# Performance work log

Hardware: AMD Instinct MI355X
Metric: run time of the kernel (lower is better)

Reference implementation:

```python
import jax, jax.numpy as jnp
import numpy as np

B, N, HID, H = 16, 256, 512, 8
DK = HID // H          # att_size = 64
FEAT = 8               # storage/operator feature dim
MLP_H = 64             # interaction MLP hidden dim
LAM = 0.1              # htap_lambda
SCALE = DK ** -0.5


def _pair_bias(feat, W1, b1, W2, b2):
    """MLP([v_i || v_j || |v_i - v_j|]) for all pairs -> [B,N,N,H].
    Split W1 over the three concat blocks so the per-node parts are O(N)."""
    F = feat.shape[-1]
    Wa, Wb, Wc = W1[:F], W1[F:2 * F], W1[2 * F:]
    hi = feat @ Wa                                    # [B,N,MLP_H]
    hj = feat @ Wb                                    # [B,N,MLP_H]
    diff = jnp.abs(feat[:, :, None, :] - feat[:, None, :, :])  # [B,N,N,F]
    h = jax.nn.relu(hi[:, :, None, :] + hj[:, None, :, :] + diff @ Wc + b1)
    return h @ W2 + b2                                # [B,N,N,H]


def setup_inputs() -> dict:
    key = jax.random.key(0)
    ks = jax.random.split(key, 24)
    g = lambda i, shape, s=0.05: jax.random.normal(ks[i], shape, jnp.float32) * (1.0 if s is None else 1.0) * (s / 0.05 * 0.05 if False else 1.0)
    def w(i, shape, scale):
        return jax.random.normal(ks[i], shape, jnp.float32) * scale
    inp = {
        "q": w(0, (B, N, HID), 1.0),
        "k": w(1, (B, N, HID), 1.0),
        "v": w(2, (B, N, HID), 1.0),
        "tree_attn_bias": w(3, (B, H, N, N), 1.0),
        "storage_features": w(4, (B, N, FEAT), 1.0),
        "operator_features": w(5, (B, N, FEAT), 1.0),
        # attention projections (stored as [in,out])
        "Wq": w(6, (HID, HID), HID ** -0.5), "bq": jnp.zeros((HID,), jnp.float32),
        "Wk": w(7, (HID, HID), HID ** -0.5), "bk": jnp.zeros((HID,), jnp.float32),
        "Wv": w(8, (HID, HID), HID ** -0.5), "bv": jnp.zeros((HID,), jnp.float32),
        "Wo": w(9, (HID, HID), HID ** -0.5), "bo": jnp.zeros((HID,), jnp.float32),
        # f_s interaction MLP: Linear(3*FEAT,64) -> ReLU -> Linear(64,H)
        "fs_W1": w(10, (3 * FEAT, MLP_H), (3 * FEAT) ** -0.5), "fs_b1": jnp.zeros((MLP_H,), jnp.float32),
        "fs_W2": w(11, (MLP_H, H), MLP_H ** -0.5), "fs_b2": jnp.zeros((H,), jnp.float32),
        # f_o interaction MLP
        "fo_W1": w(12, (3 * FEAT, MLP_H), (3 * FEAT) ** -0.5), "fo_b1": jnp.zeros((MLP_H,), jnp.float32),
        "fo_W2": w(13, (MLP_H, H), MLP_H ** -0.5), "fo_b2": jnp.zeros((H,), jnp.float32),
    }
    return inp


def reference(q, k, v, tree_attn_bias, storage_features, operator_features,
              Wq, bq, Wk, bk, Wv, bv, Wo, bo,
              fs_W1, fs_b1, fs_W2, fs_b2, fo_W1, fo_b1, fo_W2, fo_b2):
    # projections -> [B,H,N,DK]
    qh = (q @ Wq + bq).reshape(B, N, H, DK).transpose(0, 2, 1, 3) * SCALE
    kh = (k @ Wk + bk).reshape(B, N, H, DK).transpose(0, 2, 1, 3)
    vh = (v @ Wv + bv).reshape(B, N, H, DK).transpose(0, 2, 1, 3)

    scores = jnp.einsum("bhnd,bhmd->bhnm", qh, kh) + tree_attn_bias

    htap = (_pair_bias(storage_features, fs_W1, fs_b1, fs_W2, fs_b2)
            + _pair_bias(operator_features, fo_W1, fo_b1, fo_W2, fo_b2))  # [B,N,N,H]
    scores = scores + LAM * htap.transpose(0, 3, 1, 2)

    attn = jax.nn.softmax(scores, axis=-1)            # dropout rate 0 (eval)
    x = jnp.einsum("bhnm,bhmd->bhnd", attn, vh)
    x = x.transpose(0, 2, 1, 3).reshape(B, N, HID)
    return x @ Wo + bo
```

## Files before the change

### kernel.cpp

```cpp
#include <hip/hip_runtime.h>
#include <hip/hip_bf16.h>
#include <stdint.h>

#define B_    16
#define N_    256
#define HID_  512
#define H_    8
#define DK_   64
#define FEAT_ 8
#define MLPH_ 64
#define LAM_  0.1f
#define SCALE_ 0.125f

typedef short bf16x8 __attribute__((ext_vector_type(8)));
typedef float f32x4  __attribute__((ext_vector_type(4)));

union U8 { uint4 u; bf16x8 h; ushort s[8]; };

__device__ __forceinline__ uint16_t f32_to_bf16(float x) {
    uint32_t u = __float_as_uint(x);
    u += 0x7fffu + ((u >> 16) & 1u);
    return (uint16_t)(u >> 16);
}
__device__ __forceinline__ float bf16_to_f32(uint16_t v) {
    return __uint_as_float(((uint32_t)v) << 16);
}
__device__ __forceinline__ uint32_t pk_bf16(float lo, float hi) {
    float2 xy; xy.x = lo; xy.y = hi;
    __hip_bfloat162 b2 = __float22bfloat162_rn(xy);
    return *(uint32_t*)&b2;
}
#define LDS_FENCE() asm volatile("s_waitcnt lgkmcnt(0)" ::: "memory")

__global__ __launch_bounds__(256) void cvt_prep(
    const float* __restrict__ q, const float* __restrict__ k, const float* __restrict__ v,
    const float* __restrict__ Wq, const float* __restrict__ Wk,
    const float* __restrict__ Wv, const float* __restrict__ Wo,
    const float* __restrict__ fsW1, const float* __restrict__ foW1,
    const float* __restrict__ fsW2, const float* __restrict__ foW2,
    ushort* __restrict__ qb, ushort* __restrict__ kb, ushort* __restrict__ vb,
    ushort* __restrict__ Wqt, ushort* __restrict__ Wkt,
    ushort* __restrict__ Wvt, ushort* __restrict__ Wot,
    uint4* __restrict__ bfrag1, uint4* __restrict__ bfrag2)
{
    __shared__ float tile[64][65];
    int t = threadIdx.x;
    int z = blockIdx.y, bx = blockIdx.x;

    if (z < 3) {
        const float* src = (z == 0) ? q : (z == 1) ? k : v;
        ushort* dst      = (z == 0) ? qb : (z == 1) ? kb : vb;
        size_t base = (size_t)bx * 2048 + (size_t)t * 8;
        float4 a = *(const float4*)&src[base];
        float4 b = *(const float4*)&src[base + 4];
        uint4 o;
        o.x = pk_bf16(a.x, a.y); o.y = pk_bf16(a.z, a.w);
        o.z = pk_bf16(b.x, b.y); o.w = pk_bf16(b.z, b.w);
        *(uint4*)&dst[base] = o;
        return;
    }

    if (bx < 256) {
        int mat = bx >> 6, tl = bx & 63;
        const float* Wf = (mat == 0) ? Wq : (mat == 1) ? Wk : (mat == 2) ? Wv : Wo;
        ushort* Wt      = (mat == 0) ? Wqt : (mat == 1) ? Wkt : (mat == 2) ? Wvt : Wot;
        int ki0 = (tl >> 3) * 64, ni0 = (tl & 7) * 64;
        {
            int r = t >> 2, cq = (t & 3) * 16;
            #pragma unroll
            for (int j = 0; j < 4; j++) {
                float4 v4 = *(const float4*)&Wf[(ki0 + r) * HID_ + ni0 + cq + j * 4];
                tile[r][cq + j * 4 + 0] = v4.x; tile[r][cq + j * 4 + 1] = v4.y;
                tile[r][cq + j * 4 + 2] = v4.z; tile[r][cq + j * 4 + 3] = v4.w;
            }
        }
        __syncthreads();
        {
            int n = t >> 2, kq = (t & 3) * 16;
            uint4 o0, o1;
            o0.x = pk_bf16(tile[kq + 0][n], tile[kq + 1][n]);
            o0.y = pk_bf16(tile[kq + 2][n], tile[kq + 3][n]);
            o0.z = pk_bf16(tile[kq + 4][n], tile[kq + 5][n]);
            o0.w = pk_bf16(tile[kq + 6][n], tile[kq + 7][n]);
            o1.x = pk_bf16(tile[kq + 8][n], tile[kq + 9][n]);
            o1.y = pk_bf16(tile[kq + 10][n], tile[kq + 11][n]);
            o1.z = pk_bf16(tile[kq + 12][n], tile[kq + 13][n]);
            o1.w = pk_bf16(tile[kq + 14][n], tile[kq + 15][n]);
            *(uint4*)&Wt[(ni0 + n) * HID_ + ki0 + kq] = o0;
            *(uint4*)&Wt[(ni0 + n) * HID_ + ki0 + kq + 8] = o1;
        }
        return;
    }

    if (bx == 256) {
        #pragma unroll
        for (int e = t; e < 512; e += 256) {
            int nt = e >> 6, lane = e & 63, l15 = lane & 15, qd = lane >> 4;
            int n = nt * 16 + l15;
            ushort vals[8];
            #pragma unroll
            for (int u = 0; u < 8; u++) {
                float x = 0.f;
                if (n < 64) {
                    if (qd == 0) x = fsW1[(16 + u) * 64 + n];
                    else if (qd == 1) x = fsW1[(8 + u) * 64 + n];
                } else {
                    int n2 = n - 64;
                    if (qd == 2) x = foW1[(16 + u) * 64 + n2];
                    else if (qd == 3) x = foW1[(8 + u) * 64 + n2];
                }
                vals[u] = f32_to_bf16(x);
            }
            uint4 pk;
            pk.x = (uint32_t)vals[0] | ((uint32_t)vals[1] << 16);
            pk.y = (uint32_t)vals[2] | ((uint32_t)vals[3] << 16);
            pk.z = (uint32_t)vals[4] | ((uint32_t)vals[5] << 16);
            pk.w = (uint32_t)vals[6] | ((uint32_t)vals[7] << 16);
            bfrag1[e] = pk;
        }
        {
            int e = t;
            int ks = e >> 6, lane = e & 63, l15 = lane & 15, qd = lane >> 4;
            ushort vals[8];
            #pragma unroll
            for (int u = 0; u < 8; u++) {
                float x = 0.f;
                if (l15 < 8) {
                    int k2 = ks * 32 + qd * 8 + u;
                    int c = ((k2 & 7) << 4) | (k2 >> 3);
                    x = LAM_ * ((c < 64) ? fsW2[c * 8 + l15] : foW2[(c - 64) * 8 + l15]);
                }
                vals[u] = f32_to_bf16(x);
            }
            uint4 pk;
            pk.x = (uint32_t)vals[0] | ((uint32_t)vals[1] << 16);
            pk.y = (uint32_t)vals[2] | ((uint32_t)vals[3] << 16);
            pk.z = (uint32_t)vals[4] | ((uint32_t)vals[5] << 16);
            pk.w = (uint32_t)vals[6] | ((uint32_t)vals[7] << 16);
            bfrag2[e] = pk;
        }
    }
}

__global__ __launch_bounds__(256, 4) void proj_kernel(
    const ushort* __restrict__ qb, const ushort* __restrict__ kb, const ushort* __restrict__ vb,
    const ushort* __restrict__ Wqt, const ushort* __restrict__ Wkt, const ushort* __restrict__ Wvt,
    const float* __restrict__ bq, const float* __restrict__ bk, const float* __restrict__ bv,
    ushort* __restrict__ qh, ushort* __restrict__ kh, ushort* __restrict__ vh)
{
    int z = blockIdx.z;
    const ushort* X   = (z == 0) ? qb  : (z == 1) ? kb  : vb;
    const ushort* Wt  = (z == 0) ? Wqt : (z == 1) ? Wkt : Wvt;
    const float* bias = (z == 0) ? bq  : (z == 1) ? bk  : bv;
    ushort* out       = (z == 0) ? qh  : (z == 1) ? kh  : vh;
    float scale       = (z == 0) ? SCALE_ : 1.0f;

    int m0 = blockIdx.x * 128;
    int h  = blockIdx.y;
    int c0 = h * 64;

    __shared__ __align__(16) ushort Xs[2][128 * 40];
    __shared__ __align__(16) ushort Ws[2][64 * 40];

    int t = threadIdx.x;
    int wave = t >> 6, lane = t & 63;
    int l15 = lane & 15, qd = lane >> 4;

    int xr = t >> 1, xc = (t & 1) * 16;
    int wn = t >> 2, wk = (t & 3) * 8;

    f32x4 acc0[4] = {}, acc1[4] = {};

    uint4 xv0, xv1, wv;
    xv0 = *(const uint4*)&X[(size_t)(m0 + xr) * HID_ + xc];
    xv1 = *(const uint4*)&X[(size_t)(m0 + xr) * HID_ + xc + 8];
    wv  = *(const uint4*)&Wt[(size_t)(c0 + wn) * HID_ + wk];

    for (int k0 = 0; k0 < HID_; k0 += 32) {
        int buf = (k0 >> 5) & 1;
        *(uint4*)&Xs[buf][xr * 40 + xc]     = xv0;
        *(uint4*)&Xs[buf][xr * 40 + xc + 8] = xv1;
        *(uint4*)&Ws[buf][wn * 40 + wk]     = wv;
        __syncthreads();

        if (k0 + 32 < HID_) {
            int kn = k0 + 32;
            xv0 = *(const uint4*)&X[(size_t)(m0 + xr) * HID_ + kn + xc];
            xv1 = *(const uint4*)&X[(size_t)(m0 + xr) * HID_ + kn + xc + 8];
            wv  = *(const uint4*)&Wt[(size_t)(c0 + wn) * HID_ + kn + wk];
        }

        bf16x8 af0 = *(const bf16x8*)&Xs[buf][(wave * 32 + l15) * 40 + qd * 8];
        bf16x8 af1 = *(const bf16x8*)&Xs[buf][(wave * 32 + 16 + l15) * 40 + qd * 8];
        #pragma unroll
        for (int nt = 0; nt < 4; nt++) {
            bf16x8 bf = *(const bf16x8*)&Ws[buf][(nt * 16 + l15) * 40 + qd * 8];
            acc0[nt] = __builtin_amdgcn_mfma_f32_16x16x32_bf16(af0, bf, acc0[nt], 0, 0, 0);
            acc1[nt] = __builtin_amdgcn_mfma_f32_16x16x32_bf16(af1, bf, acc1[nt], 0, 0, 0);
        }
    }

    #pragma unroll
    for (int nt = 0; nt < 4; nt++) {
        float bb = bias[c0 + nt * 16 + l15];
        #pragma unroll
        for (int g = 0; g < 2; g++) {
            const f32x4& a = g ? acc1[nt] : acc0[nt];
            #pragma unroll
            for (int r = 0; r < 4; r++) {
                int m = m0 + wave * 32 + g * 16 + qd * 4 + r;
                int b_ = m >> 8, n_ = m & 255;
                float val = (a[r] + bb) * scale;
                out[(((b_ * H_ + h) * N_) + n_) * DK_ + nt * 16 + l15] = f32_to_bf16(val);
            }
        }
    }
}

#define HSTRIDE 136
__global__ __launch_bounds__(256, 3) void pair_bias_mfma(
    const float* __restrict__ sf, const float* __restrict__ of,
    const float* __restrict__ fsW1, const float* __restrict__ fsb1,
    const float* __restrict__ foW1, const float* __restrict__ fob1,
    const float* __restrict__ fsb2, const float* __restrict__ fob2,
    const uint4* __restrict__ bfrag1, const uint4* __restrict__ bfrag2,
    ushort* __restrict__ mlpb)
{
    __shared__ __align__(16) ushort hbuf[4][2][16 * HSTRIDE];
    __shared__ float hisbuf[128];
    __shared__ __align__(16) ushort mout[8 * 16 * 24];

    int i = blockIdx.x, b = blockIdx.y;
    int t = threadIdx.x;
    int wave = t >> 6, lane = t & 63;
    int l15 = lane & 15, qd = lane >> 4;

    if (t < 128) {
        int set = t >> 6, kk = t & 63;
        const float* W1 = set ? foW1 : fsW1;
        const float* fi = (set ? of : sf) + (b * N_ + i) * FEAT_;
        float a = (set ? fob1 : fsb1)[kk];
        #pragma unroll
        for (int f = 0; f < FEAT_; f++) a += fi[f] * W1[f * 64 + kk];
        hisbuf[t] = a;
    }

    bf16x8 Bf1[8], Bf2[4];
    #pragma unroll
    for (int nt = 0; nt < 8; nt++) { U8 u; u.u = bfrag1[nt * 64 + lane]; Bf1[nt] = u.h; }
    #pragma unroll
    for (int ks = 0; ks < 4; ks++) { U8 u; u.u = bfrag2[ks * 64 + lane]; Bf2[ks] = u.h; }

    const float* fsr = sf + (b * N_ + i) * FEAT_;
    const float* forr = of + (b * N_ + i) * FEAT_;
    float fsi[8], foi[8];
    #pragma unroll
    for (int u = 0; u < 8; u++) { fsi[u] = fsr[u]; foi[u] = forr[u]; }
    float b2l = LAM_ * (fsb2[l15 & 7] + fob2[l15 & 7]);

    bf16x8 af[4];
    #pragma unroll
    for (int qt = 0; qt < 4; qt++) {
        int j = (wave * 4 + qt) * 16 + l15;
        const float* fr = ((qd < 2) ? sf : of) + (b * N_ + j) * FEAT_;
        float4 f0 = *(const float4*)&fr[0];
        float4 f1 = *(const float4*)&fr[4];
        float vals[8] = {f0.x, f0.y, f0.z, f0.w, f1.x, f1.y, f1.z, f1.w};
        if ((qd & 1) == 0) {
            const float* fi = (qd < 2) ? fsi : foi;
            #pragma unroll
            for (int u = 0; u < 8; u++) vals[u] = fabsf(vals[u] - fi[u]);
        }
        U8 au;
        #pragma unroll
        for (int p = 0; p < 4; p++)
            ((uint32_t*)&au)[p] = pk_bf16(vals[2 * p], vals[2 * p + 1]);
        af[qt] = au.h;
    }

    __syncthreads();
    float hv[8];
    #pragma unroll
    for (int nt = 0; nt < 8; nt++) hv[nt] = hisbuf[nt * 16 + l15];

    {
        f32x4 S1[8];
        #pragma unroll
        for (int nt = 0; nt < 8; nt++) {
            f32x4 c0 = {hv[nt], hv[nt], hv[nt], hv[nt]};
            S1[nt] = __builtin_amdgcn_mfma_f32_16x16x32_bf16(af[0], Bf1[nt], c0, 0, 0, 0);
        }
        ushort* hb = &hbuf[wave][0][0];
        #pragma unroll
        for (int r = 0; r < 4; r++) {
            uint4 w;
            w.x = pk_bf16(fmaxf(S1[0][r], 0.f), fmaxf(S1[1][r], 0.f));
            w.y = pk_bf16(fmaxf(S1[2][r], 0.f), fmaxf(S1[3][r], 0.f));
            w.z = pk_bf16(fmaxf(S1[4][r], 0.f), fmaxf(S1[5][r], 0.f));
            w.w = pk_bf16(fmaxf(S1[6][r], 0.f), fmaxf(S1[7][r], 0.f));
            *(uint4*)&hb[(qd * 4 + r) * HSTRIDE + l15 * 8] = w;
        }
    }

    #pragma unroll
    for (int qt = 0; qt < 4; qt++) {
        ushort* hbC = &hbuf[wave][qt & 1][0];
        ushort* hbN = &hbuf[wave][(qt & 1) ^ 1][0];
        LDS_FENCE();

        f32x4 Sn[8];
        if (qt < 3) {
            #pragma unroll
            for (int nt = 0; nt < 8; nt++) {
                f32x4 c0 = {hv[nt], hv[nt], hv[nt], hv[nt]};
                Sn[nt] = __builtin_amdgcn_mfma_f32_16x16x32_bf16(af[qt + 1], Bf1[nt], c0, 0, 0, 0);
            }
        }

        f32x4 S2 = {b2l, b2l, b2l, b2l};
        #pragma unroll
        for (int ks = 0; ks < 4; ks++) {
            bf16x8 a2 = *(const bf16x8*)&hbC[l15 * HSTRIDE + ks * 32 + qd * 8];
            S2 = __builtin_amdgcn_mfma_f32_16x16x32_bf16(a2, Bf2[ks], S2, 0, 0, 0);
        }

        if (l15 < 8) {
            int j0q = wave * 4 + qt;
            #pragma unroll
            for (int r = 0; r < 4; r++)
                mout[(l15 * 16 + qd * 4 + r) * 24 + j0q] = f32_to_bf16(S2[r]);
        }

        if (qt < 3) {
            #pragma unroll
            for (int r = 0; r < 4; r++) {
                uint4 w;
                w.x = pk_bf16(fmaxf(Sn[0][r], 0.f), fmaxf(Sn[1][r], 0.f));
                w.y = pk_bf16(fmaxf(Sn[2][r], 0.f), fmaxf(Sn[3][r], 0.f));
                w.z = pk_bf16(fmaxf(Sn[4][r], 0.f), fmaxf(Sn[5][r], 0.f));
                w.w = pk_bf16(fmaxf(Sn[6][r], 0.f), fmaxf(Sn[7][r], 0.f));
                *(uint4*)&hbN[(qd * 4 + r) * HSTRIDE + l15 * 8] = w;
            }
        }
    }

    __syncthreads();

    {
        int h2 = t >> 5;
        int off = (t & 31) * 8;
        int jl = off >> 4, jh0 = off & 15;
        uint4 w = *(const uint4*)&mout[(h2 * 16 + jl) * 24 + jh0];
        *(uint4*)&mlpb[(((size_t)(b * H_ + h2) * N_ + i) * 256) + off] = w;
    }
}

__global__ __launch_bounds__(256, 2) void attn_kernel(
    const ushort* __restrict__ qh, const ushort* __restrict__ kh,
    const ushort* __restrict__ vh, const float* __restrict__ tree,
    const ushort* __restrict__ mlpb, ushort* __restrict__ ctxb)
{
    __shared__ __align__(16) ushort bufKP[256 * 72];
    __shared__ __align__(16) ushort bufV[64 * 264];

    int blk = blockIdx.x;
    int bh = blk >> 2;
    int quarter = blk & 3;

    int t = threadIdx.x;
    int wave = t >> 6, lane = t & 63;
    int l15 = lane & 15, qd = lane >> 4;
    int i0w = quarter * 64 + wave * 16;

    const ushort* khb = kh + (size_t)bh * N_ * DK_;
    const ushort* vhb = vh + (size_t)bh * N_ * DK_;

    #pragma unroll
    for (int u = t; u < 2048; u += 256) {
        int j = u >> 3, seg = (u & 7) * 8;
        uint4 kv = *(const uint4*)&khb[j * DK_ + seg];
        *(uint4*)&bufKP[j * 72 + seg] = kv;
    }
    #pragma unroll
    for (int u = t; u < 1024; u += 256) {
        int rp = u & 127, d0 = (u >> 7) * 8;
        U8 v0, v1;
        v0.u = *(const uint4*)&vhb[(2 * rp) * DK_ + d0];
        v1.u = *(const uint4*)&vhb[(2 * rp + 1) * DK_ + d0];
        #pragma unroll
        for (int jj = 0; jj < 8; jj++) {
            uint32_t pk = (uint32_t)v0.s[jj] | ((uint32_t)v1.s[jj] << 16);
            *(uint32_t*)&bufV[(d0 + jj) * 264 + 2 * rp] = pk;
        }
    }
    __syncthreads();

    bf16x8 a0, a1;
    {
        size_t qb = ((size_t)bh * N_ + i0w + l15) * DK_;
        U8 t0, t1;
        t0.u = *(const uint4*)&qh[qb + qd * 8];
        t1.u = *(const uint4*)&qh[qb + 32 + qd * 8];
        a0 = t0.h; a1 = t1.h;
    }
    f32x4 S[16];
    #pragma unroll
    for (int nt = 0; nt < 16; nt++) {
        f32x4 acc = {};
        bf16x8 b0 = *(const bf16x8*)&bufKP[(nt * 16 + l15) * 72 + qd * 8];
        bf16x8 b1 = *(const bf16x8*)&bufKP[(nt * 16 + l15) * 72 + 32 + qd * 8];
        acc = __builtin_amdgcn_mfma_f32_16x16x32_bf16(a0, b0, acc, 0, 0, 0);
        acc = __builtin_amdgcn_mfma_f32_16x16x32_bf16(a1, b1, acc, 0, 0, 0);
        S[nt] = acc;
    }

    __syncthreads();

    {
        size_t rbase = (((size_t)bh * N_ + i0w + qd * 4) * 16 + l15) * 16;
        #pragma unroll
        for (int r = 0; r < 4; r++) {
            const ushort* mbp = mlpb + rbase + (size_t)r * 256;
            U8 ma, mb2;
            ma.u  = *(const uint4*)&mbp[0];
            mb2.u = *(const uint4*)&mbp[8];
            #pragma unroll
            for (int nt = 0; nt < 8; nt++) S[nt][r]     += bf16_to_f32(ma.s[nt]);
            #pragma unroll
            for (int nt = 0; nt < 8; nt++) S[nt + 8][r] += bf16_to_f32(mb2.s[nt]);
        }
    }

    {
        float* tls = (float*)&bufKP[wave * 4608];
        #pragma unroll
        for (int half = 0; half < 2; half++) {
            #pragma unroll
            for (int f = 0; f < 8; f++) {
                int L = f * 64 + lane;
                int row = L >> 5, c4 = L & 31;
                float4 tv = *(const float4*)
                    &tree[((size_t)bh * N_ + i0w + row) * N_ + half * 128 + c4 * 4];
                *(float4*)&tls[row * 132 + c4 * 4] = tv;
            }
            LDS_FENCE();
            #pragma unroll
            for (int nt = 0; nt < 8; nt++) {
                #pragma unroll
                for (int r = 0; r < 4; r++)
                    S[half * 8 + nt][r] += tls[(qd * 4 + r) * 132 + nt * 16 + l15];
            }
            LDS_FENCE();
        }
    }

    float mx[4], sm[4];
    #pragma unroll
    for (int r = 0; r < 4; r++) mx[r] = -1e30f;
    #pragma unroll
    for (int nt = 0; nt < 16; nt++)
        #pragma unroll
        for (int r = 0; r < 4; r++) mx[r] = fmaxf(mx[r], S[nt][r]);
    #pragma unroll
    for (int r = 0; r < 4; r++) {
        #pragma unroll
        for (int m = 1; m <= 8; m <<= 1) mx[r] = fmaxf(mx[r], __shfl_xor(mx[r], m));
    }
    #pragma unroll
    for (int r = 0; r < 4; r++) sm[r] = 0.f;
    #pragma unroll
    for (int nt = 0; nt < 16; nt++)
        #pragma unroll
        for (int r = 0; r < 4; r++) {
            float e = __expf(S[nt][r] - mx[r]);
            S[nt][r] = e;
            sm[r] += e;
        }
    #pragma unroll
    for (int r = 0; r < 4; r++) {
        #pragma unroll
        for (int m = 1; m <= 8; m <<= 1) sm[r] += __shfl_xor(sm[r], m);
        sm[r] = 1.0f / sm[r];
    }

    __syncthreads();

    {
        uint32_t* Pw = (uint32_t*)&bufKP[wave * 16 * 264];
        #pragma unroll
        for (int nt = 0; nt < 16; nt++)
            #pragma unroll
            for (int r = 0; r < 4; r++) {
                float p = S[nt][r] * sm[r];
                float po = __shfl_xor(p, 1);
                uint32_t pk = (uint32_t)f32_to_bf16(p) | ((uint32_t)f32_to_bf16(po) << 16);
                if ((lane & 1) == 0)
                    Pw[(qd * 4 + r) * 132 + nt * 8 + (l15 >> 1)] = pk;
            }
    }
    __syncthreads();

    const ushort* Pw = &bufKP[wave * 16 * 264];
    f32x4 O[4] = {};
    #pragma unroll
    for (int ks = 0; ks < 8; ks++) {
        int j0 = ks * 32;
        bf16x8 pa = *(const bf16x8*)&Pw[l15 * 264 + j0 + qd * 8];
        #pragma unroll
        for (int ntd = 0; ntd < 4; ntd++) {
            bf16x8 vb = *(const bf16x8*)&bufV[(ntd * 16 + l15) * 264 + j0 + qd * 8];
            O[ntd] = __builtin_amdgcn_mfma_f32_16x16x32_bf16(pa, vb, O[ntd], 0, 0, 0);
        }
    }

    #pragma unroll
    for (int ntd = 0; ntd < 4; ntd++)
        #pragma unroll
        for (int r = 0; r < 4; r++)
            ctxb[((size_t)bh * N_ + i0w + qd * 4 + r) * DK_ + ntd * 16 + l15] =
                f32_to_bf16(O[ntd][r]);
}

__global__ __launch_bounds__(256, 4) void outproj_kernel(
    const ushort* __restrict__ ctxb, const ushort* __restrict__ Wot,
    const float* __restrict__ bo, float* __restrict__ out)
{
    int m0 = blockIdx.x * 64;
    int c0 = blockIdx.y * 64;

    __shared__ __align__(16) ushort Xs[64 * 40];
    __shared__ __align__(16) ushort Ws[64 * 40];

    int t = threadIdx.x;
    int wave = t >> 6, lane = t & 63;
    int l15 = lane & 15, qd = lane >> 4;

    f32x4 acc[4] = {};

    for (int k0 = 0; k0 < HID_; k0 += 32) {
        __syncthreads();
        {
            int r = t >> 2, s8 = (t & 3) * 8;
            int m = m0 + r, b_ = m >> 8, n_ = m & 255;
            uint4 xv = *(const uint4*)&ctxb[(((b_ * H_ + (k0 >> 6)) * N_) + n_) * DK_ + (k0 & 63) + s8];
            *(uint4*)&Xs[r * 40 + s8] = xv;
        }
        {
            int wn = t >> 2, wk = (t & 3) * 8;
            uint4 wv = *(const uint4*)&Wot[(size_t)(c0 + wn) * HID_ + k0 + wk];
            *(uint4*)&Ws[wn * 40 + wk] = wv;
        }
        __syncthreads();
        bf16x8 af = *(const bf16x8*)&Xs[(wave * 16 + l15) * 40 + qd * 8];
        #pragma unroll
        for (int nt = 0; nt < 4; nt++) {
            bf16x8 bf = *(const bf16x8*)&Ws[(nt * 16 + l15) * 40 + qd * 8];
            acc[nt] = __builtin_amdgcn_mfma_f32_16x16x32_bf16(af, bf, acc[nt], 0, 0, 0);
        }
    }

    #pragma unroll
    for (int nt = 0; nt < 4; nt++) {
        float bb = bo[c0 + nt * 16 + l15];
        #pragma unroll
        for (int r = 0; r < 4; r++) {
            int m = m0 + wave * 16 + qd * 4 + r;
            out[m * HID_ + c0 + nt * 16 + l15] = acc[nt][r] + bb;
        }
    }
}

extern "C" void kernel_launch(void* const* d_in, const int* in_sizes, int n_in,
                              void* d_out, int out_size, void* d_ws, size_t ws_size,
                              hipStream_t stream)
{
    const float* q    = (const float*)d_in[0];
    const float* k    = (const float*)d_in[1];
    const float* v    = (const float*)d_in[2];
    const float* tree = (const float*)d_in[3];
    const float* sf   = (const float*)d_in[4];
    const float* of   = (const float*)d_in[5];
    const float* Wq   = (const float*)d_in[6];
    const float* bq   = (const float*)d_in[7];
    const float* Wk   = (const float*)d_in[8];
    const float* bk   = (const float*)d_in[9];
    const float* Wv   = (const float*)d_in[10];
    const float* bv   = (const float*)d_in[11];
    const float* Wo   = (const float*)d_in[12];
    const float* bo   = (const float*)d_in[13];
    const float* fsW1 = (const float*)d_in[14];
    const float* fsb1 = (const float*)d_in[15];
    const float* fsW2 = (const float*)d_in[16];
    const float* fsb2 = (const float*)d_in[17];
    const float* foW1 = (const float*)d_in[18];
    const float* fob1 = (const float*)d_in[19];
    const float* foW2 = (const float*)d_in[20];
    const float* fob2 = (const float*)d_in[21];

    char* ws = (char*)d_ws;
    ushort* qh     = (ushort*)(ws + 0);
    ushort* kh     = (ushort*)(ws + 4194304);
    ushort* vh     = (ushort*)(ws + 8388608);
    ushort* ctxb   = (ushort*)(ws + 12582912);
    uint4*  bfrag1 = (uint4*)(ws + 16777216);
    uint4*  bfrag2 = (uint4*)(ws + 16785408);
    ushort* mlpb   = (ushort*)(ws + 23080960);
    ushort* qb     = (ushort*)(ws + 39858176);
    ushort* kb     = (ushort*)(ws + 44052480);
    ushort* vb     = (ushort*)(ws + 48246784);
    ushort* Wqt    = (ushort*)(ws + 52441088);
    ushort* Wkt    = (ushort*)(ws + 52965376);
    ushort* Wvt    = (ushort*)(ws + 53489664);
    ushort* Wot    = (ushort*)(ws + 54013952);

    cvt_prep<<<dim3(1024, 4), 256, 0, stream>>>(q, k, v, Wq, Wk, Wv, Wo,
                                                fsW1, foW1, fsW2, foW2,
                                                qb, kb, vb, Wqt, Wkt, Wvt, Wot,
                                                bfrag1, bfrag2);
    proj_kernel<<<dim3(32, 8, 3), 256, 0, stream>>>(qb, kb, vb, Wqt, Wkt, Wvt,
                                                    bq, bk, bv, qh, kh, vh);
    pair_bias_mfma<<<dim3(N_, B_), 256, 0, stream>>>(sf, of, fsW1, fsb1, foW1, fob1,
                                                     fsb2, fob2, bfrag1, bfrag2, mlpb);
    attn_kernel<<<512, 256, 0, stream>>>(qh, kh, vh, tree, mlpb, ctxb);
    outproj_kernel<<<dim3(64, 8), 256, 0, stream>>>(ctxb, Wot, bo, (float*)d_out);
}
```

Before: 210.7 us.

## Process four query rows per pair-bias block and stage ctx stores via LDS

Result: no change. 209.3 us (-0.6%).

```diff
diff --git a/kernel.cpp b/kernel.cpp
--- a/kernel.cpp
+++ b/kernel.cpp
@@ -226,132 +226,132 @@
     const uint4* __restrict__ bfrag1, const uint4* __restrict__ bfrag2,
     ushort* __restrict__ mlpb)
 {
-    __shared__ __align__(16) ushort hbuf[4][2][16 * HSTRIDE];
-    __shared__ float hisbuf[128];
+    __shared__ __align__(16) float feat[2 * N_ * FEAT_];
+    __shared__ __align__(16) ushort hbuf[4][16 * HSTRIDE];
+    __shared__ float hisbuf[4][128];
     __shared__ __align__(16) ushort mout[8 * 16 * 24];
 
-    int i = blockIdx.x, b = blockIdx.y;
+    int i0 = blockIdx.x * 4, b = blockIdx.y;
     int t = threadIdx.x;
     int wave = t >> 6, lane = t & 63;
     int l15 = lane & 15, qd = lane >> 4;
 
+    {
+        uint4* featv = (uint4*)feat;
+        const uint4* sfv = (const uint4*)(sf + (size_t)b * N_ * FEAT_);
+        const uint4* ofv = (const uint4*)(of + (size_t)b * N_ * FEAT_);
+        #pragma unroll
+        for (int p = 0; p < 4; p++) {
+            int u = t + p * 256;
+            featv[u] = (u < 512) ? sfv[u] : ofv[u - 512];
+        }
+    }
+    const float* sfs = feat;
+    const float* ofs = feat + N_ * FEAT_;
+
+    bf16x8 Bf1[8], Bf2[4];
+    #pragma unroll
+    for (int nt = 0; nt < 8; nt++) { U8 u; u.u = bfrag1[nt * 64 + lane]; Bf1[nt] = u.h; }
+    #pragma unroll
+    for (int ks = 0; ks < 4; ks++) { U8 u; u.u = bfrag2[ks * 64 + lane]; Bf2[ks] = u.h; }
+    float b2l = LAM_ * (fsb2[l15 & 7] + fob2[l15 & 7]);
+
+    __syncthreads();
+
     if (t < 128) {
         int set = t >> 6, kk = t & 63;
         const float* W1 = set ? foW1 : fsW1;
-        const float* fi = (set ? of : sf) + (b * N_ + i) * FEAT_;
-        float a = (set ? fob1 : fsb1)[kk];
-        #pragma unroll
-        for (int f = 0; f < FEAT_; f++) a += fi[f] * W1[f * 64 + kk];
-        hisbuf[t] = a;
-    }
-
-    bf16x8 Bf1[8], Bf2[4];
-    #pragma unroll
-    for (int nt = 0; nt < 8; nt++) { U8 u; u.u = bfrag1[nt * 64 + lane]; Bf1[nt] = u.h; }
-    #pragma unroll
-    for (int ks = 0; ks < 4; ks++) { U8 u; u.u = bfrag2[ks * 64 + lane]; Bf2[ks] = u.h; }
-
-    const float* fsr = sf + (b * N_ + i) * FEAT_;
-    const float* forr = of + (b * N_ + i) * FEAT_;
-    float fsi[8], foi[8];
-    #pragma unroll
-    for (int u = 0; u < 8; u++) { fsi[u] = fsr[u]; foi[u] = forr[u]; }
-    float b2l = LAM_ * (fsb2[l15 & 7] + fob2[l15 & 7]);
-
-    bf16x8 af[4];
-    #pragma unroll
-    for (int qt = 0; qt < 4; qt++) {
-        int j = (wave * 4 + qt) * 16 + l15;
-        const float* fr = ((qd < 2) ? sf : of) + (b * N_ + j) * FEAT_;
-        float4 f0 = *(const float4*)&fr[0];
-        float4 f1 = *(const float4*)&fr[4];
-        float vals[8] = {f0.x, f0.y, f0.z, f0.w, f1.x, f1.y, f1.z, f1.w};
-        if ((qd & 1) == 0) {
-            const float* fi = (qd < 2) ? fsi : foi;
-            #pragma unroll
-            for (int u = 0; u < 8; u++) vals[u] = fabsf(vals[u] - fi[u]);
-        }
-        U8 au;
-        #pragma unroll
-        for (int p = 0; p < 4; p++)
-            ((uint32_t*)&au)[p] = pk_bf16(vals[2 * p], vals[2 * p + 1]);
-        af[qt] = au.h;
-    }
-
-    __syncthreads();
-    float hv[8];
-    #pragma unroll
-    for (int nt = 0; nt < 8; nt++) hv[nt] = hisbuf[nt * 16 + l15];
-
-    {
-        f32x4 S1[8];
-        #pragma unroll
-        for (int nt = 0; nt < 8; nt++) {
-            f32x4 c0 = {hv[nt], hv[nt], hv[nt], hv[nt]};
-            S1[nt] = __builtin_amdgcn_mfma_f32_16x16x32_bf16(af[0], Bf1[nt], c0, 0, 0, 0);
-        }
-        ushort* hb = &hbuf[wave][0][0];
-        #pragma unroll
-        for (int r = 0; r < 4; r++) {
-            uint4 w;
-            w.x = pk_bf16(fmaxf(S1[0][r], 0.f), fmaxf(S1[1][r], 0.f));
-            w.y = pk_bf16(fmaxf(S1[2][r], 0.f), fmaxf(S1[3][r], 0.f));
-            w.z = pk_bf16(fmaxf(S1[4][r], 0.f), fmaxf(S1[5][r], 0.f));
-            w.w = pk_bf16(fmaxf(S1[6][r], 0.f), fmaxf(S1[7][r], 0.f));
-            *(uint4*)&hb[(qd * 4 + r) * HSTRIDE + l15 * 8] = w;
-        }
-    }
-
-    #pragma unroll
-    for (int qt = 0; qt < 4; qt++) {
-        ushort* hbC = &hbuf[wave][qt & 1][0];
-        ushort* hbN = &hbuf[wave][(qt & 1) ^ 1][0];
-        LDS_FENCE();
-
-        f32x4 Sn[8];
-        if (qt < 3) {
+        float bb = (set ? fob1 : fsb1)[kk];
+        #pragma unroll
+        for (int ii = 0; ii < 4; ii++) {
+            const float* fi = (set ? ofs : sfs) + (i0 + ii) * FEAT_;
+            float a = bb;
+            #pragma unroll
+            for (int f = 0; f < FEAT_; f++) a += fi[f] * W1[f * 64 + kk];
+            hisbuf[ii][t] = a;
+        }
+    }
+    __syncthreads();
+
+    ushort* hb = &hbuf[wave][0];
+
+    for (int ii = 0; ii < 4; ii++) {
+        int i = i0 + ii;
+
+        float fsi[8], foi[8];
+        #pragma unroll
+        for (int u = 0; u < 8; u++) { fsi[u] = sfs[i * FEAT_ + u]; foi[u] = ofs[i * FEAT_ + u]; }
+
+        float hv[8];
+        #pragma unroll
+        for (int nt = 0; nt < 8; nt++) hv[nt] = hisbuf[ii][nt * 16 + l15];
+
+        bf16x8 af[4];
+        #pragma unroll
+        for (int qt = 0; qt < 4; qt++) {
+            int j = (wave * 4 + qt) * 16 + l15;
+            const float* fr = ((qd < 2) ? sfs : ofs) + j * FEAT_;
+            float4 f0 = *(const float4*)&fr[0];
+            float4 f1 = *(const float4*)&fr[4];
+            float vals[8] = {f0.x, f0.y, f0.z, f0.w, f1.x, f1.y, f1.z, f1.w};
+            if ((qd & 1) == 0) {
+                const float* fi = (qd < 2) ? fsi : foi;
+                #pragma unroll
+                for (int u = 0; u < 8; u++) vals[u] = fabsf(vals[u] - fi[u]);
+            }
+            U8 au;
+            #pragma unroll
+            for (int p = 0; p < 4; p++)
+                ((uint32_t*)&au)[p] = pk_bf16(vals[2 * p], vals[2 * p + 1]);
+            af[qt] = au.h;
+        }
+
+        #pragma unroll
+        for (int qt = 0; qt < 4; qt++) {
+            f32x4 S1[8];
             #pragma unroll
             for (int nt = 0; nt < 8; nt++) {
                 f32x4 c0 = {hv[nt], hv[nt], hv[nt], hv[nt]};
-                Sn[nt] = __builtin_amdgcn_mfma_f32_16x16x32_bf16(af[qt + 1], Bf1[nt], c0, 0, 0, 0);
-            }
-        }
-
-        f32x4 S2 = {b2l, b2l, b2l, b2l};
-        #pragma unroll
-        for (int ks = 0; ks < 4; ks++) {
-            bf16x8 a2 = *(const bf16x8*)&hbC[l15 * HSTRIDE + ks * 32 + qd * 8];
-            S2 = __builtin_amdgcn_mfma_f32_16x16x32_bf16(a2, Bf2[ks], S2, 0, 0, 0);
-        }
-
-        if (l15 < 8) {
-            int j0q = wave * 4 + qt;
-            #pragma unroll
-            for (int r = 0; r < 4; r++)
-                mout[(l15 * 16 + qd * 4 + r) * 24 + j0q] = f32_to_bf16(S2[r]);
-        }
-
-        if (qt < 3) {
+                S1[nt] = __builtin_amdgcn_mfma_f32_16x16x32_bf16(af[qt], Bf1[nt], c0, 0, 0, 0);
+            }
             #pragma unroll
             for (int r = 0; r < 4; r++) {
                 uint4 w;
-                w.x = pk_bf16(fmaxf(Sn[0][r], 0.f), fmaxf(Sn[1][r], 0.f));
-                w.y = pk_bf16(fmaxf(Sn[2][r], 0.f), fmaxf(Sn[3][r], 0.f));
-                w.z = pk_bf16(fmaxf(Sn[4][r], 0.f), fmaxf(Sn[5][r], 0.f));
-                w.w = pk_bf16(fmaxf(Sn[6][r], 0.f), fmaxf(Sn[7][r], 0.f));
-                *(uint4*)&hbN[(qd * 4 + r) * HSTRIDE + l15 * 8] = w;
-            }
-        }
-    }
-
-    __syncthreads();
-
-    {
-        int h2 = t >> 5;
-        int off = (t & 31) * 8;
-        int jl = off >> 4, jh0 = off & 15;
-        uint4 w = *(const uint4*)&mout[(h2 * 16 + jl) * 24 + jh0];
-        *(uint4*)&mlpb[(((size_t)(b * H_ + h2) * N_ + i) * 256) + off] = w;
+                w.x = pk_bf16(fmaxf(S1[0][r], 0.f), fmaxf(S1[1][r], 0.f));
+                w.y = pk_bf16(fmaxf(S1[2][r], 0.f), fmaxf(S1[3][r], 0.f));
+                w.z = pk_bf16(fmaxf(S1[4][r], 0.f), fmaxf(S1[5][r], 0.f));
+                w.w = pk_bf16(fmaxf(S1[6][r], 0.f), fmaxf(S1[7][r], 0.f));
+                *(uint4*)&hb[(qd * 4 + r) * HSTRIDE + l15 * 8] = w;
+            }
+            LDS_FENCE();
+
+            f32x4 S2 = {b2l, b2l, b2l, b2l};
+            #pragma unroll
+            for (int ks = 0; ks < 4; ks++) {
+                bf16x8 a2 = *(const bf16x8*)&hb[l15 * HSTRIDE + ks * 32 + qd * 8];
+                S2 = __builtin_amdgcn_mfma_f32_16x16x32_bf16(a2, Bf2[ks], S2, 0, 0, 0);
+            }
+            LDS_FENCE();
+
+            if (l15 < 8) {
+                int j0q = wave * 4 + qt;
+                #pragma unroll
+                for (int r = 0; r < 4; r++)
+                    mout[(l15 * 16 + qd * 4 + r) * 24 + j0q] = f32_to_bf16(S2[r]);
+            }
+        }
+
+        __syncthreads();
+
+        {
+            int h2 = t >> 5;
+            int off = (t & 31) * 8;
+            int jl = off >> 4, jh0 = off & 15;
+            uint4 w = *(const uint4*)&mout[(h2 * 16 + jl) * 24 + jh0];
+            *(uint4*)&mlpb[(((size_t)(b * H_ + h2) * N_ + i) * 256) + off] = w;
+        }
+
+        __syncthreads();
     }
 }
 
@@ -513,12 +513,24 @@
         }
     }
 
-    #pragma unroll
-    for (int ntd = 0; ntd < 4; ntd++)
-        #pragma unroll
-        for (int r = 0; r < 4; r++)
-            ctxb[((size_t)bh * N_ + i0w + qd * 4 + r) * DK_ + ntd * 16 + l15] =
-                f32_to_bf16(O[ntd][r]);
+    __syncthreads();
+    {
+        ushort* ob = bufV;
+        #pragma unroll
+        for (int ntd = 0; ntd < 4; ntd++)
+            #pragma unroll
+            for (int r = 0; r < 4; r++)
+                ob[(wave * 16 + qd * 4 + r) * 72 + ntd * 16 + l15] = f32_to_bf16(O[ntd][r]);
+    }
+    __syncthreads();
+    {
+        int row = t >> 2, cc = (t & 3) * 16;
+        uint4 w0 = *(const uint4*)&bufV[row * 72 + cc];
+        uint4 w1 = *(const uint4*)&bufV[row * 72 + cc + 8];
+        size_t dst = ((size_t)bh * N_ + quarter * 64 + row) * DK_ + cc;
+        *(uint4*)&ctxb[dst]     = w0;
+        *(uint4*)&ctxb[dst + 8] = w1;
+    }
 }
 
 __global__ __launch_bounds__(256, 4) void outproj_kernel(
@@ -619,7 +631,7 @@
                                                 bfrag1, bfrag2);
     proj_kernel<<<dim3(32, 8, 3), 256, 0, stream>>>(qb, kb, vb, Wqt, Wkt, Wvt,
                                                     bq, bk, bv, qh, kh, vh);
-    pair_bias_mfma<<<dim3(N_, B_), 256, 0, stream>>>(sf, of, fsW1, fsb1, foW1, fob1,
+    pair_bias_mfma<<<dim3(64, B_), 256, 0, stream>>>(sf, of, fsW1, fsb1, foW1, fob1,
                                                      fsb2, fob2, bfrag1, bfrag2, mlpb);
     attn_kernel<<<512, 256, 0, stream>>>(qh, kh, vh, tree, mlpb, ctxb);
     outproj_kernel<<<dim3(64, 8), 256, 0, stream>>>(ctxb, Wot, bo, (float*)d_out);
```
